# Optimization experiments

Hardware: AMD Instinct MI355X
Metric: run time of the kernel (lower is better)

Reference implementation:

```python
import jax, jax.numpy as jnp
import numpy as np
from jax import lax


def setup_inputs() -> dict:
    key = jax.random.key(0)
    ks = jax.random.split(key, 5)
    D, S, T, B, H = 2, 48, 48, 32, 256
    std = 1.0 / np.sqrt(H)
    return {
        "src_input_seq": jax.random.normal(ks[0], (S, B, H), jnp.float32),
        "trg_input_seq": jax.random.normal(ks[1], (T, B, H), jnp.float32),
        "W": jax.random.uniform(ks[2], (D, H, H), jnp.float32, -std, std),
        "U": jax.random.uniform(ks[3], (D, 2 * H, H), jnp.float32, -std, std),
        "b": jax.random.uniform(ks[4], (D, 1, H), jnp.float32, -std, std),
    }


def _grid_layer(x, y, Wd, Ud, bd):
    # x, y: [S, T, B, H] per-cell inputs for this depth
    S, T, B, H = x.shape
    Ux, Uy = Ud[:H], Ud[H:]  # state = concat([state_x, state_y]) @ U

    def row_step(prev_row_hx, row_inputs):
        # prev_row_hx: [T, B, H] = h_x of row i-1 (state_x); zeros for i == 0
        x_row, y_row = row_inputs  # [T, B, H]

        def cell_step(left_hx, inp):
            # left_hx: [B, H] = h_x of cell (i, j-1) (state_y); zeros for j == 0
            up_hx, x_t, y_t = inp
            temp = up_hx @ Ux + left_hx @ Uy + bd  # [B, H]
            h_x = jnp.tanh(x_t @ Wd + temp)
            h_y = jnp.tanh(y_t @ Wd + temp)
            return h_x, (h_x, h_y)

        _, (hx_row, hy_row) = lax.scan(
            cell_step, jnp.zeros((B, H), x.dtype), (prev_row_hx, x_row, y_row)
        )
        return hx_row, (hx_row, hy_row)

    _, (HX, HY) = lax.scan(row_step, jnp.zeros((T, B, H), x.dtype), (x, y))
    return jnp.stack([HX, HY], axis=2)  # [S, T, 2, B, H]


def reference(src_input_seq, trg_input_seq, W, U, b):
    S, B, H = src_input_seq.shape
    T = trg_input_seq.shape[0]
    depth = W.shape[0]
    # depth-0 inputs: x_t = src[i] (same for all j), y_t = trg[j] (same for all i)
    xs = jnp.broadcast_to(src_input_seq[:, None], (S, T, B, H))
    ys = jnp.broadcast_to(trg_input_seq[None, :], (S, T, B, H))
    outs = []
    for d in range(depth):
        Hd = _grid_layer(xs, ys, W[d], U[d], b[d])  # [S, T, 2, B, H]
        outs.append(Hd)
        xs, ys = Hd[:, :, 0], Hd[:, :, 1]
    return jnp.stack(outs, axis=0)  # [depth, S, T, 2, B, H]
```

## Files before the change

kernel.cpp:

```cpp
#include <hip/hip_runtime.h>
#include <hip/hip_bf16.h>


typedef short short8 __attribute__((ext_vector_type(8)));
typedef float f32x4 __attribute__((ext_vector_type(4)));

static constexpr size_t UF_OFF    = 0;
static constexpr size_t WF_OFF    = 512u * 1024;
static constexpr size_t SRCW_OFF  = 768u * 1024;
static constexpr size_t TRGW_OFF  = SRCW_OFF + 48u * 32 * 256 * 4;
static constexpr size_t FLAG0_OFF = TRGW_OFF + 48u * 32 * 256 * 4;
static constexpr size_t FLAG1_OFF = FLAG0_OFF + 48u * 48 * 128;
static constexpr int    FSTRIDE   = 32;

#define MFMA16(a, b, c) __builtin_amdgcn_mfma_f32_16x16x32_bf16(a, b, c, 0, 0, 0)

__device__ __forceinline__ short f2bf(float f) {
  __hip_bfloat16 h = __float2bfloat16(f);
  return __builtin_bit_cast(short, h);
}

__device__ __forceinline__ size_t plane_off(int d, int s, int t, int c) {
  return (size_t)(((d * 48 + s) * 48 + t) * 2 + c) * 8192u;
}

__device__ __forceinline__ void wait_ge(int* p, int v) {
  while (__hip_atomic_load(p, __ATOMIC_RELAXED, __HIP_MEMORY_SCOPE_AGENT) < v)
    __builtin_amdgcn_s_sleep(1);
  asm volatile("" ::: "memory");
}

__device__ __forceinline__ void st_llc(float* p, float v) {
  __hip_atomic_store(p, v, __ATOMIC_RELAXED, __HIP_MEMORY_SCOPE_AGENT);
}

__device__ __forceinline__ float fast_tanh(float x) {
  float e = exp2f(x * 2.88539008f);
  return 1.f - __fdividef(2.f, e + 1.f);
}

__global__ void preswizzle(const float* __restrict__ U,
                           const float* __restrict__ W,
                           char* __restrict__ ws) {
  int gid = blockIdx.x * 256 + threadIdx.x;
  if (gid < 32768) {
    int r = gid >> 11;
    int d = r >> 3, nh = (r >> 2) & 1, w = r & 3;
    int c = gid & 2047;
    int f = c >> 6, lane = c & 63;
    int nt = f >> 4, ks = f & 15;
    int kbase = ks * 32 + (lane >> 4) * 8;
    int n = nh * 128 + w * 32 + nt * 16 + (lane & 15);
    const float* sp = U + (size_t)d * 512 * 256 + n;
    short8 v;
#pragma unroll
    for (int j = 0; j < 8; ++j) v[j] = f2bf(sp[(size_t)(kbase + j) * 256]);
    *(short8*)(ws + UF_OFF + (size_t)gid * 16) = v;
  } else {
    int idx = gid - 32768;
    int r = idx >> 10;
    int d = r >> 3, nh = (r >> 2) & 1, w = r & 3;
    int c = idx & 1023;
    int f = c >> 6, lane = c & 63;
    int nt = f >> 3, ks = f & 7;
    int kbase = ks * 32 + (lane >> 4) * 8;
    int n = nh * 128 + w * 32 + nt * 16 + (lane & 15);
    const float* sp = W + (size_t)d * 256 * 256 + n;
    short8 v;
#pragma unroll
    for (int j = 0; j < 8; ++j) v[j] = f2bf(sp[(size_t)(kbase + j) * 256]);
    *(short8*)(ws + WF_OFF + (size_t)idx * 16) = v;
  }
}

__global__ __launch_bounds__(256, 1) void precompute_xw(
    const float* __restrict__ src, const float* __restrict__ trg,
    const float* __restrict__ bvec, char* __restrict__ ws) {
  __shared__ __align__(16) char lds[32 * 528];
  const int bid = blockIdx.x;
  const int i = bid >> 1, nh = bid & 1;
  const int tid = threadIdx.x;
  const int w = tid >> 6, lane = tid & 63;
  const int alane = lane & 15, q = lane >> 4;

  short8 bw[2][8];
  {
    const char* wb = ws + WF_OFF + (size_t)(nh * 4 + w) * 16384u + (size_t)lane * 16;
#pragma unroll
    for (int nt = 0; nt < 2; ++nt)
#pragma unroll
      for (int ks = 0; ks < 8; ++ks)
        bw[nt][ks] = *(const short8*)(wb + (nt * 8 + ks) * 1024);
  }

  const float* plane = (i < 48) ? src + (size_t)i * 8192 : trg + (size_t)(i - 48) * 8192;
#pragma unroll
  for (int it = 0; it < 4; ++it) {
    int gid = it * 256 + tid;
    int row = gid >> 5, c = gid & 31;
    const float* p = plane + row * 256 + c * 8;
    short8 v;
#pragma unroll
    for (int j = 0; j < 8; ++j) v[j] = f2bf(p[j]);
    *(short8*)(lds + row * 528 + c * 16) = v;
  }
  __syncthreads();

  const f32x4 zf = {0.f, 0.f, 0.f, 0.f};
  f32x4 acc[2][2];
  acc[0][0] = zf; acc[0][1] = zf; acc[1][0] = zf; acc[1][1] = zf;
  const char* ar0 = lds + alane * 528 + q * 16;
  const char* ar1 = lds + (alane + 16) * 528 + q * 16;
#pragma unroll
  for (int ks = 0; ks < 8; ++ks) {
    short8 a0 = *(const short8*)(ar0 + ks * 64);
    short8 a1 = *(const short8*)(ar1 + ks * 64);
#pragma unroll
    for (int nt = 0; nt < 2; ++nt) {
      acc[0][nt] = MFMA16(a0, bw[nt][ks], acc[0][nt]);
      acc[1][nt] = MFMA16(a1, bw[nt][ks], acc[1][nt]);
    }
  }

  const int n0 = nh * 128 + w * 32 + alane;
  float bs[2] = {bvec[n0], bvec[n0 + 16]};
  float* dst = (float*)(ws + (i < 48 ? SRCW_OFF : TRGW_OFF)) +
               (size_t)(i < 48 ? i : i - 48) * 8192;
#pragma unroll
  for (int mt = 0; mt < 2; ++mt)
#pragma unroll
    for (int nt = 0; nt < 2; ++nt)
#pragma unroll
      for (int rr = 0; rr < 4; ++rr) {
        int row = mt * 16 + q * 4 + rr;
        dst[row * 256 + n0 + nt * 16] = acc[mt][nt][rr] + bs[nt];
      }
}

__global__ __launch_bounds__(512, 2) void grid_main(
    float* __restrict__ out, const float* __restrict__ bvec,
    char* __restrict__ ws) {
  __shared__ __align__(16) char lds[3 * 32 * 528];
  char* const buf0 = lds;
  char* const buf1 = lds + 32 * 528;
  char* const buf2 = lds + 2 * 32 * 528;

  const int bid = blockIdx.x;
  const int d = bid / 48;
  const int t = bid % 48;
  const int tid = threadIdx.x;
  const int wv = tid >> 6;
  const int nh = wv >> 2, w = wv & 3;
  const int lane = tid & 63;
  const int alane = lane & 15, q = lane >> 4;
  const int n0 = nh * 128 + w * 32 + alane;

  int* flag0 = (int*)(ws + FLAG0_OFF);
  int* flag1 = (int*)(ws + FLAG1_OFF);
  const float* SRCW = (const float*)(ws + SRCW_OFF);
  const float* TRGW = (const float*)(ws + TRGW_OFF);

  for (int i = tid; i < 32 * 528 / 4; i += 512) ((int*)buf0)[i] = 0;

  short8 bu[2][16];
  {
    const char* ub = ws + UF_OFF + (size_t)((d * 2 + nh) * 4 + w) * 32768u +
                     (size_t)lane * 16;
#pragma unroll
    for (int nt = 0; nt < 2; ++nt)
#pragma unroll
      for (int ks = 0; ks < 16; ++ks)
        bu[nt][ks] = *(const short8*)(ub + (nt * 16 + ks) * 1024);
  }

  const char* up0 = buf0 + alane * 528 + q * 16;
  const char* up1 = buf0 + (alane + 16) * 528 + q * 16;
  const char* l0  = buf1 + alane * 528 + q * 16;
  const char* l1  = buf1 + (alane + 16) * 528 + q * 16;
  const char* y0  = buf2 + alane * 528 + q * 16;
  const char* y1  = buf2 + (alane + 16) * 528 + q * 16;

  __syncthreads();

  if (d == 0) {
    float pfy[16];
    {
      const float* syp = TRGW + (size_t)t * 8192;
#pragma unroll
      for (int mt = 0; mt < 2; ++mt)
#pragma unroll
        for (int nt = 0; nt < 2; ++nt)
#pragma unroll
          for (int rr = 0; rr < 4; ++rr) {
            int row = mt * 16 + q * 4 + rr;
            pfy[(mt * 2 + nt) * 4 + rr] = syp[row * 256 + n0 + nt * 16];
          }
    }
    for (int s = 0; s < 48; ++s) {
      f32x4 accx[2][2], accy[2][2];
      {
        const float* sxp = SRCW + (size_t)s * 8192;
#pragma unroll
        for (int mt = 0; mt < 2; ++mt)
#pragma unroll
          for (int nt = 0; nt < 2; ++nt)
#pragma unroll
            for (int rr = 0; rr < 4; ++rr) {
              int row = mt * 16 + q * 4 + rr;
              accx[mt][nt][rr] = sxp[row * 256 + n0 + nt * 16];
              accy[mt][nt][rr] = pfy[(mt * 2 + nt) * 4 + rr];
            }
      }
      if (t > 0) {
        wait_ge(&flag0[(s * 48 + (t - 1)) * FSTRIDE], 8);
        const float* pl = out + plane_off(0, s, t - 1, 0);
#pragma unroll
        for (int it = 0; it < 2; ++it) {
          int gid = it * 512 + tid;
          int row = gid >> 5, c = gid & 31;
          const float* p = pl + row * 256 + c * 8;
          short8 v;
#pragma unroll
          for (int j = 0; j < 8; ++j) v[j] = f2bf(p[j]);
          *(short8*)(buf1 + row * 528 + c * 16) = v;
        }
      }
      __syncthreads();
#pragma unroll
      for (int ks = 0; ks < 8; ++ks) {
        short8 a0 = *(const short8*)(up0 + ks * 64);
        short8 a1 = *(const short8*)(up1 + ks * 64);
        accx[0][0] = MFMA16(a0, bu[0][ks], accx[0][0]);
        accx[0][1] = MFMA16(a0, bu[1][ks], accx[0][1]);
        accx[1][0] = MFMA16(a1, bu[0][ks], accx[1][0]);
        accx[1][1] = MFMA16(a1, bu[1][ks], accx[1][1]);
        accy[0][0] = MFMA16(a0, bu[0][ks], accy[0][0]);
        accy[0][1] = MFMA16(a0, bu[1][ks], accy[0][1]);
        accy[1][0] = MFMA16(a1, bu[0][ks], accy[1][0]);
        accy[1][1] = MFMA16(a1, bu[1][ks], accy[1][1]);
      }
      if (t > 0) {
#pragma unroll
        for (int ks = 0; ks < 8; ++ks) {
          short8 a0 = *(const short8*)(l0 + ks * 64);
          short8 a1 = *(const short8*)(l1 + ks * 64);
          accx[0][0] = MFMA16(a0, bu[0][8 + ks], accx[0][0]);
          accx[0][1] = MFMA16(a0, bu[1][8 + ks], accx[0][1]);
          accx[1][0] = MFMA16(a1, bu[0][8 + ks], accx[1][0]);
          accx[1][1] = MFMA16(a1, bu[1][8 + ks], accx[1][1]);
          accy[0][0] = MFMA16(a0, bu[0][8 + ks], accy[0][0]);
          accy[0][1] = MFMA16(a0, bu[1][8 + ks], accy[0][1]);
          accy[1][0] = MFMA16(a1, bu[0][8 + ks], accy[1][0]);
          accy[1][1] = MFMA16(a1, bu[1][8 + ks], accy[1][1]);
        }
      }
      float hx[16];
      {
        float* hxp = out + plane_off(0, s, t, 0);
        float* hyp = out + plane_off(0, s, t, 1);
#pragma unroll
        for (int mt = 0; mt < 2; ++mt)
#pragma unroll
          for (int nt = 0; nt < 2; ++nt)
#pragma unroll
            for (int rr = 0; rr < 4; ++rr) {
              int row = mt * 16 + q * 4 + rr;
              int n = n0 + nt * 16;
              float xv = fast_tanh(accx[mt][nt][rr]);
              float yv = fast_tanh(accy[mt][nt][rr]);
              hx[(mt * 2 + nt) * 4 + rr] = xv;
              st_llc(&hxp[row * 256 + n], xv);
              st_llc(&hyp[row * 256 + n], yv);
            }
      }
      asm volatile("s_waitcnt vmcnt(0)" ::: "memory");
      if (lane == 0)
        __hip_atomic_fetch_add(&flag0[(s * 48 + t) * FSTRIDE], 1,
                               __ATOMIC_RELAXED, __HIP_MEMORY_SCOPE_AGENT);
      __syncthreads();
#pragma unroll
      for (int mt = 0; mt < 2; ++mt)
#pragma unroll
        for (int nt = 0; nt < 2; ++nt)
#pragma unroll
          for (int rr = 0; rr < 4; ++rr) {
            int row = mt * 16 + q * 4 + rr;
            *(short*)(buf0 + row * 528 + (n0 + nt * 16) * 2) =
                f2bf(hx[(mt * 2 + nt) * 4 + rr]);
          }
      __syncthreads();
    }
  } else {
    const char* wb = ws + WF_OFF + (size_t)((2 + nh) * 4 + w) * 16384u +
                     (size_t)lane * 16;
    const float bsa = bvec[256 + n0], bsb = bvec[256 + n0 + 16];
    const f32x4 bA = {bsa, bsa, bsa, bsa};
    const f32x4 bB = {bsb, bsb, bsb, bsb};
    const f32x4 zf = {0.f, 0.f, 0.f, 0.f};
    for (int s = 0; s < 48; ++s) {
      f32x4 accx[2][2], accy[2][2], acc[2][2];
      accx[0][0] = bA; accx[0][1] = bB; accx[1][0] = bA; accx[1][1] = bB;
      accy[0][0] = bA; accy[0][1] = bB; accy[1][0] = bA; accy[1][1] = bB;
      acc[0][0] = zf; acc[0][1] = zf; acc[1][0] = zf; acc[1][1] = zf;

      wait_ge(&flag0[(s * 48 + t) * FSTRIDE], 8);
      {
        const float* px = out + plane_off(0, s, t, 0);
        const float* py = out + plane_off(0, s, t, 1);
#pragma unroll
        for (int it = 0; it < 4; ++it) {
          int gid = it * 512 + tid;
          int pidx = gid >> 10, row = (gid >> 5) & 31, c = gid & 31;
          const float* pp = pidx ? py : px;
          char* db = pidx ? buf2 : buf1;
          const float* p = pp + row * 256 + c * 8;
          short8 v;
#pragma unroll
          for (int j = 0; j < 8; ++j) v[j] = f2bf(p[j]);
          *(short8*)(db + row * 528 + c * 16) = v;
        }
      }
      __syncthreads();
#pragma unroll
      for (int ks = 0; ks < 8; ++ks) {
        short8 b0 = *(const short8*)(wb + ks * 1024);
        short8 b1 = *(const short8*)(wb + (8 + ks) * 1024);
        short8 ax0 = *(const short8*)(l0 + ks * 64);
        short8 ax1 = *(const short8*)(l1 + ks * 64);
        short8 ay0 = *(const short8*)(y0 + ks * 64);
        short8 ay1 = *(const short8*)(y1 + ks * 64);
        accx[0][0] = MFMA16(ax0, b0, accx[0][0]);
        accx[0][1] = MFMA16(ax0, b1, accx[0][1]);
        accx[1][0] = MFMA16(ax1, b0, accx[1][0]);
        accx[1][1] = MFMA16(ax1, b1, accx[1][1]);
        accy[0][0] = MFMA16(ay0, b0, accy[0][0]);
        accy[0][1] = MFMA16(ay0, b1, accy[0][1]);
        accy[1][0] = MFMA16(ay1, b0, accy[1][0]);
        accy[1][1] = MFMA16(ay1, b1, accy[1][1]);
      }
      if (t > 0) wait_ge(&flag1[(s * 48 + (t - 1)) * FSTRIDE], 8);
      __syncthreads();
      if (t > 0) {
        const float* pl = out + plane_off(1, s, t - 1, 0);
#pragma unroll
        for (int it = 0; it < 2; ++it) {
          int gid = it * 512 + tid;
          int row = gid >> 5, c = gid & 31;
          const float* p = pl + row * 256 + c * 8;
          short8 v;
#pragma unroll
          for (int j = 0; j < 8; ++j) v[j] = f2bf(p[j]);
          *(short8*)(buf1 + row * 528 + c * 16) = v;
        }
      }
      __syncthreads();
#pragma unroll
      for (int ks = 0; ks < 8; ++ks) {
        short8 a0 = *(const short8*)(up0 + ks * 64);
        short8 a1 = *(const short8*)(up1 + ks * 64);
        acc[0][0] = MFMA16(a0, bu[0][ks], acc[0][0]);
        acc[0][1] = MFMA16(a0, bu[1][ks], acc[0][1]);
        acc[1][0] = MFMA16(a1, bu[0][ks], acc[1][0]);
        acc[1][1] = MFMA16(a1, bu[1][ks], acc[1][1]);
      }
      if (t > 0) {
#pragma unroll
        for (int ks = 0; ks < 8; ++ks) {
          short8 a0 = *(const short8*)(l0 + ks * 64);
          short8 a1 = *(const short8*)(l1 + ks * 64);
          acc[0][0] = MFMA16(a0, bu[0][8 + ks], acc[0][0]);
          acc[0][1] = MFMA16(a0, bu[1][8 + ks], acc[0][1]);
          acc[1][0] = MFMA16(a1, bu[0][8 + ks], acc[1][0]);
          acc[1][1] = MFMA16(a1, bu[1][8 + ks], acc[1][1]);
        }
      }
      float hx[16];
      {
        float* hxp = out + plane_off(1, s, t, 0);
        float* hyp = out + plane_off(1, s, t, 1);
#pragma unroll
        for (int mt = 0; mt < 2; ++mt)
#pragma unroll
          for (int nt = 0; nt < 2; ++nt)
#pragma unroll
            for (int rr = 0; rr < 4; ++rr) {
              int row = mt * 16 + q * 4 + rr;
              int n = n0 + nt * 16;
              float tv = acc[mt][nt][rr];
              float xv = fast_tanh(accx[mt][nt][rr] + tv);
              float yv = fast_tanh(accy[mt][nt][rr] + tv);
              hx[(mt * 2 + nt) * 4 + rr] = xv;
              st_llc(&hxp[row * 256 + n], xv);
              hyp[row * 256 + n] = yv;
            }
      }
      asm volatile("s_waitcnt vmcnt(0)" ::: "memory");
      if (lane == 0)
        __hip_atomic_fetch_add(&flag1[(s * 48 + t) * FSTRIDE], 1,
                               __ATOMIC_RELAXED, __HIP_MEMORY_SCOPE_AGENT);
      __syncthreads();
#pragma unroll
      for (int mt = 0; mt < 2; ++mt)
#pragma unroll
        for (int nt = 0; nt < 2; ++nt)
#pragma unroll
          for (int rr = 0; rr < 4; ++rr) {
            int row = mt * 16 + q * 4 + rr;
            *(short*)(buf0 + row * 528 + (n0 + nt * 16) * 2) =
                f2bf(hx[(mt * 2 + nt) * 4 + rr]);
          }
      __syncthreads();
    }
  }
}

extern "C" void kernel_launch(void* const* d_in, const int* in_sizes, int n_in,
                              void* d_out, int out_size, void* d_ws, size_t ws_size,
                              hipStream_t stream) {
  const float* src = (const float*)d_in[0];
  const float* trg = (const float*)d_in[1];
  const float* W   = (const float*)d_in[2];
  const float* U   = (const float*)d_in[3];
  const float* bv  = (const float*)d_in[4];
  float* out = (float*)d_out;
  char* ws = (char*)d_ws;

  hipMemsetAsync(ws + FLAG0_OFF, 0, 2u * 48 * 48 * 128, stream);
  preswizzle<<<192, 256, 0, stream>>>(U, W, ws);
  precompute_xw<<<192, 256, 0, stream>>>(src, trg, bv, ws);
  grid_main<<<96, 512, 0, stream>>>(out, bv, ws);
}
```

Measured before the change: 901.8 us.

## Exchange cross-block hidden states via bf16 ring staging buffers in MFMA fragment layout

Blocks now publish h_x/h_y as bf16 into ring-buffered staging areas (8 slots per column) in workspace, and neighbours read them straight into MFMA A-fragments with atomic loads. This replaces reading fp32 output planes, converting them and bouncing them through LDS with extra barriers. The depth-0 path computes a shared temp accumulator once instead of duplicating MFMAs for x and y. U/W fragments are loaded from memory per step instead of being held in registers, and src/trg projections are stored in fragment order for vector loads. Ring reuse needs extra back-pressure waits on the consumers' flags, and the per-step weight reloads may add memory latency on the serial critical path.

```diff
diff --git a/kernel.cpp b/kernel.cpp
--- a/kernel.cpp
+++ b/kernel.cpp
@@ -4,6 +4,7 @@
 
 typedef short short8 __attribute__((ext_vector_type(8)));
 typedef float f32x4 __attribute__((ext_vector_type(4)));
+typedef int   i32x4 __attribute__((ext_vector_type(4)));
 
 static constexpr size_t UF_OFF    = 0;
 static constexpr size_t WF_OFF    = 512u * 1024;
@@ -11,7 +12,9 @@
 static constexpr size_t TRGW_OFF  = SRCW_OFF + 48u * 32 * 256 * 4;
 static constexpr size_t FLAG0_OFF = TRGW_OFF + 48u * 32 * 256 * 4;
 static constexpr size_t FLAG1_OFF = FLAG0_OFF + 48u * 48 * 128;
-static constexpr int    FSTRIDE   = 32;
+static constexpr size_t STG0X_OFF = FLAG1_OFF + 48u * 48 * 128;
+static constexpr size_t STG0Y_OFF = STG0X_OFF + 48u * 8 * 16384;
+static constexpr size_t STG1X_OFF = STG0Y_OFF + 48u * 8 * 16384;
 
 #define MFMA16(a, b, c) __builtin_amdgcn_mfma_f32_16x16x32_bf16(a, b, c, 0, 0, 0)
 
@@ -22,6 +25,10 @@
 
 __device__ __forceinline__ size_t plane_off(int d, int s, int t, int c) {
   return (size_t)(((d * 48 + s) * 48 + t) * 2 + c) * 8192u;
+}
+
+__device__ __forceinline__ int* flagp(char* ws, size_t off, int s, int t) {
+  return (int*)(ws + off) + (size_t)(s * 48 + t) * 32;
 }
 
 __device__ __forceinline__ void wait_ge(int* p, int v) {
@@ -30,8 +37,18 @@
   asm volatile("" ::: "memory");
 }
 
-__device__ __forceinline__ void st_llc(float* p, float v) {
+__device__ __forceinline__ void st_llc_u16(unsigned short* p, unsigned short v) {
   __hip_atomic_store(p, v, __ATOMIC_RELAXED, __HIP_MEMORY_SCOPE_AGENT);
+}
+
+__device__ __forceinline__ short8 ld_stg16(const char* p) {
+  const int* ip = (const int*)p;
+  i32x4 r;
+  r.x = __hip_atomic_load(ip + 0, __ATOMIC_RELAXED, __HIP_MEMORY_SCOPE_AGENT);
+  r.y = __hip_atomic_load(ip + 1, __ATOMIC_RELAXED, __HIP_MEMORY_SCOPE_AGENT);
+  r.z = __hip_atomic_load(ip + 2, __ATOMIC_RELAXED, __HIP_MEMORY_SCOPE_AGENT);
+  r.w = __hip_atomic_load(ip + 3, __ATOMIC_RELAXED, __HIP_MEMORY_SCOPE_AGENT);
+  return __builtin_bit_cast(short8, r);
 }
 
 __device__ __forceinline__ float fast_tanh(float x) {
@@ -124,26 +141,23 @@
 
   const int n0 = nh * 128 + w * 32 + alane;
   float bs[2] = {bvec[n0], bvec[n0 + 16]};
+  const int gtid = (nh * 4 + w) * 64 + lane;
   float* dst = (float*)(ws + (i < 48 ? SRCW_OFF : TRGW_OFF)) +
-               (size_t)(i < 48 ? i : i - 48) * 8192;
+               (size_t)(i < 48 ? i : i - 48) * 8192 + (size_t)gtid * 16;
 #pragma unroll
   for (int mt = 0; mt < 2; ++mt)
 #pragma unroll
-    for (int nt = 0; nt < 2; ++nt)
-#pragma unroll
-      for (int rr = 0; rr < 4; ++rr) {
-        int row = mt * 16 + q * 4 + rr;
-        dst[row * 256 + n0 + nt * 16] = acc[mt][nt][rr] + bs[nt];
-      }
+    for (int nt = 0; nt < 2; ++nt) {
+      f32x4 v = acc[mt][nt];
+      v[0] += bs[nt]; v[1] += bs[nt]; v[2] += bs[nt]; v[3] += bs[nt];
+      ((f32x4*)dst)[mt * 2 + nt] = v;
+    }
 }
 
 __global__ __launch_bounds__(512, 2) void grid_main(
     float* __restrict__ out, const float* __restrict__ bvec,
     char* __restrict__ ws) {
-  __shared__ __align__(16) char lds[3 * 32 * 528];
-  char* const buf0 = lds;
-  char* const buf1 = lds + 32 * 528;
-  char* const buf2 = lds + 2 * 32 * 528;
+  __shared__ __align__(16) char buf0[32 * 528];
 
   const int bid = blockIdx.x;
   const int d = bid / 48;
@@ -155,106 +169,110 @@
   const int alane = lane & 15, q = lane >> 4;
   const int n0 = nh * 128 + w * 32 + alane;
 
-  int* flag0 = (int*)(ws + FLAG0_OFF);
-  int* flag1 = (int*)(ws + FLAG1_OFF);
   const float* SRCW = (const float*)(ws + SRCW_OFF);
   const float* TRGW = (const float*)(ws + TRGW_OFF);
-
-  for (int i = tid; i < 32 * 528 / 4; i += 512) ((int*)buf0)[i] = 0;
-
-  short8 bu[2][16];
-  {
-    const char* ub = ws + UF_OFF + (size_t)((d * 2 + nh) * 4 + w) * 32768u +
-                     (size_t)lane * 16;
-#pragma unroll
-    for (int nt = 0; nt < 2; ++nt)
-#pragma unroll
-      for (int ks = 0; ks < 16; ++ks)
-        bu[nt][ks] = *(const short8*)(ub + (nt * 16 + ks) * 1024);
-  }
+  const char* ubp = ws + UF_OFF + (size_t)((d * 2 + nh) * 4 + w) * 32768u +
+                    (size_t)lane * 16;
+
+  for (int z = tid; z < 32 * 528 / 4; z += 512) ((int*)buf0)[z] = 0;
+  __syncthreads();
 
   const char* up0 = buf0 + alane * 528 + q * 16;
   const char* up1 = buf0 + (alane + 16) * 528 + q * 16;
-  const char* l0  = buf1 + alane * 528 + q * 16;
-  const char* l1  = buf1 + (alane + 16) * 528 + q * 16;
-  const char* y0  = buf2 + alane * 528 + q * 16;
-  const char* y1  = buf2 + (alane + 16) * 528 + q * 16;
-
-  __syncthreads();
+  const f32x4 zf = {0.f, 0.f, 0.f, 0.f};
 
   if (d == 0) {
-    float pfy[16];
+    f32x4 pfy[4];
     {
-      const float* syp = TRGW + (size_t)t * 8192;
-#pragma unroll
-      for (int mt = 0; mt < 2; ++mt)
-#pragma unroll
-        for (int nt = 0; nt < 2; ++nt)
-#pragma unroll
-          for (int rr = 0; rr < 4; ++rr) {
-            int row = mt * 16 + q * 4 + rr;
-            pfy[(mt * 2 + nt) * 4 + rr] = syp[row * 256 + n0 + nt * 16];
-          }
+      const f32x4* py = (const f32x4*)(TRGW + (size_t)t * 8192 + (size_t)tid * 16);
+      pfy[0] = py[0]; pfy[1] = py[1]; pfy[2] = py[2]; pfy[3] = py[3];
     }
     for (int s = 0; s < 48; ++s) {
-      f32x4 accx[2][2], accy[2][2];
-      {
-        const float* sxp = SRCW + (size_t)s * 8192;
-#pragma unroll
-        for (int mt = 0; mt < 2; ++mt)
-#pragma unroll
-          for (int nt = 0; nt < 2; ++nt)
-#pragma unroll
-            for (int rr = 0; rr < 4; ++rr) {
-              int row = mt * 16 + q * 4 + rr;
-              accx[mt][nt][rr] = sxp[row * 256 + n0 + nt * 16];
-              accy[mt][nt][rr] = pfy[(mt * 2 + nt) * 4 + rr];
-            }
-      }
-      if (t > 0) {
-        wait_ge(&flag0[(s * 48 + (t - 1)) * FSTRIDE], 8);
-        const float* pl = out + plane_off(0, s, t - 1, 0);
-#pragma unroll
-        for (int it = 0; it < 2; ++it) {
-          int gid = it * 512 + tid;
-          int row = gid >> 5, c = gid & 31;
-          const float* p = pl + row * 256 + c * 8;
-          short8 v;
-#pragma unroll
-          for (int j = 0; j < 8; ++j) v[j] = f2bf(p[j]);
-          *(short8*)(buf1 + row * 528 + c * 16) = v;
-        }
-      }
-      __syncthreads();
+      f32x4 accx[2][2], accy[2][2], accT[2][2];
+      {
+        const f32x4* px = (const f32x4*)(SRCW + (size_t)s * 8192 + (size_t)tid * 16);
+        accx[0][0] = px[0]; accx[0][1] = px[1]; accx[1][0] = px[2]; accx[1][1] = px[3];
+      }
+      accy[0][0] = pfy[0]; accy[0][1] = pfy[1]; accy[1][0] = pfy[2]; accy[1][1] = pfy[3];
+      accT[0][0] = zf; accT[0][1] = zf; accT[1][0] = zf; accT[1][1] = zf;
+
 #pragma unroll
       for (int ks = 0; ks < 8; ++ks) {
+        short8 b0 = *(const short8*)(ubp + (0 * 16 + ks) * 1024);
+        short8 b1 = *(const short8*)(ubp + (1 * 16 + ks) * 1024);
         short8 a0 = *(const short8*)(up0 + ks * 64);
         short8 a1 = *(const short8*)(up1 + ks * 64);
-        accx[0][0] = MFMA16(a0, bu[0][ks], accx[0][0]);
-        accx[0][1] = MFMA16(a0, bu[1][ks], accx[0][1]);
-        accx[1][0] = MFMA16(a1, bu[0][ks], accx[1][0]);
-        accx[1][1] = MFMA16(a1, bu[1][ks], accx[1][1]);
-        accy[0][0] = MFMA16(a0, bu[0][ks], accy[0][0]);
-        accy[0][1] = MFMA16(a0, bu[1][ks], accy[0][1]);
-        accy[1][0] = MFMA16(a1, bu[0][ks], accy[1][0]);
-        accy[1][1] = MFMA16(a1, bu[1][ks], accy[1][1]);
+        accT[0][0] = MFMA16(a0, b0, accT[0][0]);
+        accT[0][1] = MFMA16(a0, b1, accT[0][1]);
+        accT[1][0] = MFMA16(a1, b0, accT[1][0]);
+        accT[1][1] = MFMA16(a1, b1, accT[1][1]);
+      }
+      if (s >= 8) {
+        if (t < 47) wait_ge(flagp(ws, FLAG0_OFF, s - 8, t + 1), 8);
+        wait_ge(flagp(ws, FLAG1_OFF, s - 8, t), 8);
       }
       if (t > 0) {
-#pragma unroll
-        for (int ks = 0; ks < 8; ++ks) {
-          short8 a0 = *(const short8*)(l0 + ks * 64);
-          short8 a1 = *(const short8*)(l1 + ks * 64);
-          accx[0][0] = MFMA16(a0, bu[0][8 + ks], accx[0][0]);
-          accx[0][1] = MFMA16(a0, bu[1][8 + ks], accx[0][1]);
-          accx[1][0] = MFMA16(a1, bu[0][8 + ks], accx[1][0]);
-          accx[1][1] = MFMA16(a1, bu[1][8 + ks], accx[1][1]);
-          accy[0][0] = MFMA16(a0, bu[0][8 + ks], accy[0][0]);
-          accy[0][1] = MFMA16(a0, bu[1][8 + ks], accy[0][1]);
-          accy[1][0] = MFMA16(a1, bu[0][8 + ks], accy[1][0]);
-          accy[1][1] = MFMA16(a1, bu[1][8 + ks], accy[1][1]);
-        }
-      }
-      float hx[16];
+        wait_ge(flagp(ws, FLAG0_OFF, s, t - 1), 8);
+        const char* L = ws + STG0X_OFF + ((size_t)(t - 1) * 8 + (s & 7)) * 16384;
+        const char* p0 = L + alane * 512 + q * 16;
+        const char* p1 = L + (alane + 16) * 512 + q * 16;
+        short8 la0[8], la1[8];
+#pragma unroll
+        for (int ks = 0; ks < 8; ++ks) {
+          la0[ks] = ld_stg16(p0 + ks * 64);
+          la1[ks] = ld_stg16(p1 + ks * 64);
+        }
+#pragma unroll
+        for (int ks = 0; ks < 8; ++ks) {
+          short8 b0 = *(const short8*)(ubp + (0 * 16 + 8 + ks) * 1024);
+          short8 b1 = *(const short8*)(ubp + (1 * 16 + 8 + ks) * 1024);
+          accT[0][0] = MFMA16(la0[ks], b0, accT[0][0]);
+          accT[0][1] = MFMA16(la0[ks], b1, accT[0][1]);
+          accT[1][0] = MFMA16(la1[ks], b0, accT[1][0]);
+          accT[1][1] = MFMA16(la1[ks], b1, accT[1][1]);
+        }
+      }
+      float hxv[16], hyv[16];
+      {
+        char* SX = ws + STG0X_OFF + ((size_t)t * 8 + (s & 7)) * 16384;
+#pragma unroll
+        for (int mt = 0; mt < 2; ++mt)
+#pragma unroll
+          for (int nt = 0; nt < 2; ++nt)
+#pragma unroll
+            for (int rr = 0; rr < 4; ++rr) {
+              int i = (mt * 2 + nt) * 4 + rr;
+              int row = mt * 16 + q * 4 + rr, c = n0 + nt * 16;
+              float xv = fast_tanh(accx[mt][nt][rr] + accT[mt][nt][rr]);
+              hxv[i] = xv;
+              st_llc_u16((unsigned short*)(SX + row * 512 + c * 2),
+                         (unsigned short)f2bf(xv));
+            }
+      }
+      asm volatile("s_waitcnt vmcnt(0)" ::: "memory");
+      if (lane == 0)
+        __hip_atomic_fetch_add(flagp(ws, FLAG0_OFF, s, t), 1,
+                               __ATOMIC_RELAXED, __HIP_MEMORY_SCOPE_AGENT);
+      {
+        char* SY = ws + STG0Y_OFF + ((size_t)t * 8 + (s & 7)) * 16384;
+#pragma unroll
+        for (int mt = 0; mt < 2; ++mt)
+#pragma unroll
+          for (int nt = 0; nt < 2; ++nt)
+#pragma unroll
+            for (int rr = 0; rr < 4; ++rr) {
+              int i = (mt * 2 + nt) * 4 + rr;
+              int row = mt * 16 + q * 4 + rr, c = n0 + nt * 16;
+              float yv = fast_tanh(accy[mt][nt][rr] + accT[mt][nt][rr]);
+              hyv[i] = yv;
+              st_llc_u16((unsigned short*)(SY + row * 512 + c * 2),
+                         (unsigned short)f2bf(yv));
+            }
+      }
+      asm volatile("s_waitcnt vmcnt(0)" ::: "memory");
+      if (lane == 0)
+        __hip_atomic_fetch_add(flagp(ws, FLAG0_OFF, s, t) + 1, 1,
+                               __ATOMIC_RELAXED, __HIP_MEMORY_SCOPE_AGENT);
       {
         float* hxp = out + plane_off(0, s, t, 0);
         float* hyp = out + plane_off(0, s, t, 1);
@@ -264,19 +282,12 @@
           for (int nt = 0; nt < 2; ++nt)
 #pragma unroll
             for (int rr = 0; rr < 4; ++rr) {
-              int row = mt * 16 + q * 4 + rr;
-              int n = n0 + nt * 16;
-              float xv = fast_tanh(accx[mt][nt][rr]);
-              float yv = fast_tanh(accy[mt][nt][rr]);
-              hx[(mt * 2 + nt) * 4 + rr] = xv;
-              st_llc(&hxp[row * 256 + n], xv);
-              st_llc(&hyp[row * 256 + n], yv);
+              int i = (mt * 2 + nt) * 4 + rr;
+              int row = mt * 16 + q * 4 + rr, c = n0 + nt * 16;
+              hxp[row * 256 + c] = hxv[i];
+              hyp[row * 256 + c] = hyv[i];
             }
       }
-      asm volatile("s_waitcnt vmcnt(0)" ::: "memory");
-      if (lane == 0)
-        __hip_atomic_fetch_add(&flag0[(s * 48 + t) * FSTRIDE], 1,
-                               __ATOMIC_RELAXED, __HIP_MEMORY_SCOPE_AGENT);
       __syncthreads();
 #pragma unroll
       for (int mt = 0; mt < 2; ++mt)
@@ -284,97 +295,128 @@
         for (int nt = 0; nt < 2; ++nt)
 #pragma unroll
           for (int rr = 0; rr < 4; ++rr) {
-            int row = mt * 16 + q * 4 + rr;
-            *(short*)(buf0 + row * 528 + (n0 + nt * 16) * 2) =
-                f2bf(hx[(mt * 2 + nt) * 4 + rr]);
+            int row = mt * 16 + q * 4 + rr, c = n0 + nt * 16;
+            *(short*)(buf0 + row * 528 + c * 2) = f2bf(hxv[(mt * 2 + nt) * 4 + rr]);
           }
       __syncthreads();
     }
   } else {
-    const char* wb = ws + WF_OFF + (size_t)((2 + nh) * 4 + w) * 16384u +
-                     (size_t)lane * 16;
+    const char* wbp = ws + WF_OFF + (size_t)((2 + nh) * 4 + w) * 16384u +
+                      (size_t)lane * 16;
     const float bsa = bvec[256 + n0], bsb = bvec[256 + n0 + 16];
     const f32x4 bA = {bsa, bsa, bsa, bsa};
     const f32x4 bB = {bsb, bsb, bsb, bsb};
-    const f32x4 zf = {0.f, 0.f, 0.f, 0.f};
     for (int s = 0; s < 48; ++s) {
-      f32x4 accx[2][2], accy[2][2], acc[2][2];
+      f32x4 accx[2][2], accy[2][2], accT[2][2];
       accx[0][0] = bA; accx[0][1] = bB; accx[1][0] = bA; accx[1][1] = bB;
       accy[0][0] = bA; accy[0][1] = bB; accy[1][0] = bA; accy[1][1] = bB;
-      acc[0][0] = zf; acc[0][1] = zf; acc[1][0] = zf; acc[1][1] = zf;
-
-      wait_ge(&flag0[(s * 48 + t) * FSTRIDE], 8);
-      {
-        const float* px = out + plane_off(0, s, t, 0);
-        const float* py = out + plane_off(0, s, t, 1);
-#pragma unroll
-        for (int it = 0; it < 4; ++it) {
-          int gid = it * 512 + tid;
-          int pidx = gid >> 10, row = (gid >> 5) & 31, c = gid & 31;
-          const float* pp = pidx ? py : px;
-          char* db = pidx ? buf2 : buf1;
-          const float* p = pp + row * 256 + c * 8;
-          short8 v;
-#pragma unroll
-          for (int j = 0; j < 8; ++j) v[j] = f2bf(p[j]);
-          *(short8*)(db + row * 528 + c * 16) = v;
-        }
-      }
-      __syncthreads();
+      accT[0][0] = zf; accT[0][1] = zf; accT[1][0] = zf; accT[1][1] = zf;
+
 #pragma unroll
       for (int ks = 0; ks < 8; ++ks) {
-        short8 b0 = *(const short8*)(wb + ks * 1024);
-        short8 b1 = *(const short8*)(wb + (8 + ks) * 1024);
-        short8 ax0 = *(const short8*)(l0 + ks * 64);
-        short8 ax1 = *(const short8*)(l1 + ks * 64);
-        short8 ay0 = *(const short8*)(y0 + ks * 64);
-        short8 ay1 = *(const short8*)(y1 + ks * 64);
-        accx[0][0] = MFMA16(ax0, b0, accx[0][0]);
-        accx[0][1] = MFMA16(ax0, b1, accx[0][1]);
-        accx[1][0] = MFMA16(ax1, b0, accx[1][0]);
-        accx[1][1] = MFMA16(ax1, b1, accx[1][1]);
-        accy[0][0] = MFMA16(ay0, b0, accy[0][0]);
-        accy[0][1] = MFMA16(ay0, b1, accy[0][1]);
-        accy[1][0] = MFMA16(ay1, b0, accy[1][0]);
-        accy[1][1] = MFMA16(ay1, b1, accy[1][1]);
-      }
-      if (t > 0) wait_ge(&flag1[(s * 48 + (t - 1)) * FSTRIDE], 8);
-      __syncthreads();
-      if (t > 0) {
-        const float* pl = out + plane_off(1, s, t - 1, 0);
-#pragma unroll
-        for (int it = 0; it < 2; ++it) {
-          int gid = it * 512 + tid;
-          int row = gid >> 5, c = gid & 31;
-          const float* p = pl + row * 256 + c * 8;
-          short8 v;
-#pragma unroll
-          for (int j = 0; j < 8; ++j) v[j] = f2bf(p[j]);
-          *(short8*)(buf1 + row * 528 + c * 16) = v;
-        }
-      }
-      __syncthreads();
-#pragma unroll
-      for (int ks = 0; ks < 8; ++ks) {
+        short8 b0 = *(const short8*)(ubp + (0 * 16 + ks) * 1024);
+        short8 b1 = *(const short8*)(ubp + (1 * 16 + ks) * 1024);
         short8 a0 = *(const short8*)(up0 + ks * 64);
         short8 a1 = *(const short8*)(up1 + ks * 64);
-        acc[0][0] = MFMA16(a0, bu[0][ks], acc[0][0]);
-        acc[0][1] = MFMA16(a0, bu[1][ks], acc[0][1]);
-        acc[1][0] = MFMA16(a1, bu[0][ks], acc[1][0]);
-        acc[1][1] = MFMA16(a1, bu[1][ks], acc[1][1]);
+        accT[0][0] = MFMA16(a0, b0, accT[0][0]);
+        accT[0][1] = MFMA16(a0, b1, accT[0][1]);
+        accT[1][0] = MFMA16(a1, b0, accT[1][0]);
+        accT[1][1] = MFMA16(a1, b1, accT[1][1]);
+      }
+      if (s >= 8 && t < 47) wait_ge(flagp(ws, FLAG1_OFF, s - 8, t + 1), 8);
+
+      wait_ge(flagp(ws, FLAG0_OFF, s, t) + 1, 8);
+      {
+        const char* X = ws + STG0X_OFF + ((size_t)t * 8 + (s & 7)) * 16384;
+        const char* p0 = X + alane * 512 + q * 16;
+        const char* p1 = X + (alane + 16) * 512 + q * 16;
+        short8 ax0[8], ax1[8];
+#pragma unroll
+        for (int ks = 0; ks < 8; ++ks) {
+          ax0[ks] = ld_stg16(p0 + ks * 64);
+          ax1[ks] = ld_stg16(p1 + ks * 64);
+        }
+#pragma unroll
+        for (int ks = 0; ks < 8; ++ks) {
+          short8 b0 = *(const short8*)(wbp + ks * 1024);
+          short8 b1 = *(const short8*)(wbp + (8 + ks) * 1024);
+          accx[0][0] = MFMA16(ax0[ks], b0, accx[0][0]);
+          accx[0][1] = MFMA16(ax0[ks], b1, accx[0][1]);
+          accx[1][0] = MFMA16(ax1[ks], b0, accx[1][0]);
+          accx[1][1] = MFMA16(ax1[ks], b1, accx[1][1]);
+        }
+      }
+      {
+        const char* Y = ws + STG0Y_OFF + ((size_t)t * 8 + (s & 7)) * 16384;
+        const char* p0 = Y + alane * 512 + q * 16;
+        const char* p1 = Y + (alane + 16) * 512 + q * 16;
+        short8 ay0[8], ay1[8];
+#pragma unroll
+        for (int ks = 0; ks < 8; ++ks) {
+          ay0[ks] = ld_stg16(p0 + ks * 64);
+          ay1[ks] = ld_stg16(p1 + ks * 64);
+        }
+#pragma unroll
+        for (int ks = 0; ks < 8; ++ks) {
+          short8 b0 = *(const short8*)(wbp + ks * 1024);
+          short8 b1 = *(const short8*)(wbp + (8 + ks) * 1024);
+          accy[0][0] = MFMA16(ay0[ks], b0, accy[0][0]);
+          accy[0][1] = MFMA16(ay0[ks], b1, accy[0][1]);
+          accy[1][0] = MFMA16(ay1[ks], b0, accy[1][0]);
+          accy[1][1] = MFMA16(ay1[ks], b1, accy[1][1]);
+        }
       }
       if (t > 0) {
-#pragma unroll
-        for (int ks = 0; ks < 8; ++ks) {
-          short8 a0 = *(const short8*)(l0 + ks * 64);
-          short8 a1 = *(const short8*)(l1 + ks * 64);
-          acc[0][0] = MFMA16(a0, bu[0][8 + ks], acc[0][0]);
-          acc[0][1] = MFMA16(a0, bu[1][8 + ks], acc[0][1]);
-          acc[1][0] = MFMA16(a1, bu[0][8 + ks], acc[1][0]);
-          acc[1][1] = MFMA16(a1, bu[1][8 + ks], acc[1][1]);
-        }
-      }
-      float hx[16];
+        wait_ge(flagp(ws, FLAG1_OFF, s, t - 1), 8);
+        const char* L = ws + STG1X_OFF + ((size_t)(t - 1) * 8 + (s & 7)) * 16384;
+        const char* p0 = L + alane * 512 + q * 16;
+        const char* p1 = L + (alane + 16) * 512 + q * 16;
+        short8 la0[8], la1[8];
+#pragma unroll
+        for (int ks = 0; ks < 8; ++ks) {
+          la0[ks] = ld_stg16(p0 + ks * 64);
+          la1[ks] = ld_stg16(p1 + ks * 64);
+        }
+#pragma unroll
+        for (int ks = 0; ks < 8; ++ks) {
+          short8 b0 = *(const short8*)(ubp + (0 * 16 + 8 + ks) * 1024);
+          short8 b1 = *(const short8*)(ubp + (1 * 16 + 8 + ks) * 1024);
+          accT[0][0] = MFMA16(la0[ks], b0, accT[0][0]);
+          accT[0][1] = MFMA16(la0[ks], b1, accT[0][1]);
+          accT[1][0] = MFMA16(la1[ks], b0, accT[1][0]);
+          accT[1][1] = MFMA16(la1[ks], b1, accT[1][1]);
+        }
+      }
+      float hxv[16], hyv[16];
+      {
+        char* SX = ws + STG1X_OFF + ((size_t)t * 8 + (s & 7)) * 16384;
+#pragma unroll
+        for (int mt = 0; mt < 2; ++mt)
+#pragma unroll
+          for (int nt = 0; nt < 2; ++nt)
+#pragma unroll
+            for (int rr = 0; rr < 4; ++rr) {
+              int i = (mt * 2 + nt) * 4 + rr;
+              int row = mt * 16 + q * 4 + rr, c = n0 + nt * 16;
+              float xv = fast_tanh(accx[mt][nt][rr] + accT[mt][nt][rr]);
+              hxv[i] = xv;
+              if (t < 47)
+                st_llc_u16((unsigned short*)(SX + row * 512 + c * 2),
+                           (unsigned short)f2bf(xv));
+            }
+      }
+      asm volatile("s_waitcnt vmcnt(0)" ::: "memory");
+      if (lane == 0)
+        __hip_atomic_fetch_add(flagp(ws, FLAG1_OFF, s, t), 1,
+                               __ATOMIC_RELAXED, __HIP_MEMORY_SCOPE_AGENT);
+#pragma unroll
+      for (int mt = 0; mt < 2; ++mt)
+#pragma unroll
+        for (int nt = 0; nt < 2; ++nt)
+#pragma unroll
+          for (int rr = 0; rr < 4; ++rr)
+            hyv[(mt * 2 + nt) * 4 + rr] =
+                fast_tanh(accy[mt][nt][rr] + accT[mt][nt][rr]);
       {
         float* hxp = out + plane_off(1, s, t, 0);
         float* hyp = out + plane_off(1, s, t, 1);
@@ -384,20 +426,12 @@
           for (int nt = 0; nt < 2; ++nt)
 #pragma unroll
             for (int rr = 0; rr < 4; ++rr) {
-              int row = mt * 16 + q * 4 + rr;
-              int n = n0 + nt * 16;
-              float tv = acc[mt][nt][rr];
-              float xv = fast_tanh(accx[mt][nt][rr] + tv);
-              float yv = fast_tanh(accy[mt][nt][rr] + tv);
-              hx[(mt * 2 + nt) * 4 + rr] = xv;
-              st_llc(&hxp[row * 256 + n], xv);
-              hyp[row * 256 + n] = yv;
+              int i = (mt * 2 + nt) * 4 + rr;
+              int row = mt * 16 + q * 4 + rr, c = n0 + nt * 16;
+              hxp[row * 256 + c] = hxv[i];
+              hyp[row * 256 + c] = hyv[i];
             }
       }
-      asm volatile("s_waitcnt vmcnt(0)" ::: "memory");
-      if (lane == 0)
-        __hip_atomic_fetch_add(&flag1[(s * 48 + t) * FSTRIDE], 1,
-                               __ATOMIC_RELAXED, __HIP_MEMORY_SCOPE_AGENT);
       __syncthreads();
 #pragma unroll
       for (int mt = 0; mt < 2; ++mt)
@@ -405,9 +439,8 @@
         for (int nt = 0; nt < 2; ++nt)
 #pragma unroll
           for (int rr = 0; rr < 4; ++rr) {
-            int row = mt * 16 + q * 4 + rr;
-            *(short*)(buf0 + row * 528 + (n0 + nt * 16) * 2) =
-                f2bf(hx[(mt * 2 + nt) * 4 + rr]);
+            int row = mt * 16 + q * 4 + rr, c = n0 + nt * 16;
+            *(short*)(buf0 + row * 528 + c * 2) = f2bf(hxv[(mt * 2 + nt) * 4 + rr]);
           }
       __syncthreads();
     }
```

New measurement: 3.574 ms. +296.3%, slower.
